# Kernel optimization log

Measured on AMD Instinct MI355X. Metric: run time of the kernel, lower is better.

The kernel has to match this reference:

```python
import jax, jax.numpy as jnp
import numpy as np

LUT_DIM = 33  # standard 33^3 color LUT


def setup_inputs() -> dict:
    key = jax.random.key(0)
    k1, k2 = jax.random.split(key)
    # learned 3D LUT: [out_channels=3, D_b, D_g, D_r]
    lut = jax.random.normal(k1, (3, LUT_DIM, LUT_DIM, LUT_DIM), dtype=jnp.float32) * 0.1
    # input image batch in [0, 1): [B, 3, H, W]
    x = jax.random.uniform(k2, (4, 3, 1024, 1024), dtype=jnp.float32)
    return {"lut": lut, "x": x}


def reference(lut, x):
    """Trilinear interpolation of a 3D color LUT (image-adaptive-3DLUT forward).

    lut: [3, D, D, D] laid out as lut[c, ib, ig, ir] (flat index ir + ig*D + ib*D*D)
    x:   [B, 3, H, W] with channels (r, g, b) in [0, 1]
    returns: [B, 3, H, W]
    """
    dim = lut.shape[-1]
    scale = dim - 1  # 1 / binsize

    r, g, b = x[:, 0], x[:, 1], x[:, 2]  # each [B, H, W]

    def cell(c):
        s = c * scale
        idx = jnp.clip(jnp.floor(s), 0, scale - 1).astype(jnp.int32)
        return idx, s - idx.astype(s.dtype)  # integer cell, fractional offset

    ir, dr = cell(r)
    ig, dg = cell(g)
    ib, db = cell(b)

    lut_flat = lut.reshape(3, -1)  # [3, D^3], tiny and cache-resident

    out = jnp.zeros((3,) + r.shape, dtype=x.dtype)  # [3, B, H, W]
    # 8 corners of the enclosing LUT cell, trilinear weights
    for or_ in (0, 1):
        wr = dr if or_ else (1.0 - dr)
        for og in (0, 1):
            wg = dg if og else (1.0 - dg)
            for ob in (0, 1):
                wb = db if ob else (1.0 - db)
                flat = ((ib + ob) * dim + (ig + og)) * dim + (ir + or_)  # [B, H, W]
                corner = lut_flat[:, flat]  # gather -> [3, B, H, W]
                out = out + (wr * wg * wb)[None] * corner

    return jnp.transpose(out, (1, 0, 2, 3))  # [B, 3, H, W]
```

## Files before the change

### kernel.cpp

```cpp
#include <hip/hip_runtime.h>
#include <hip/hip_fp16.h>


#define LUT_D     33
#define LUT_DD    (LUT_D * LUT_D)
#define LUT_N     (LUT_D * LUT_D * LUT_D)
#define CH_STRIDE 35940
#define STAGE_G   (CH_STRIDE / 4)
#define HW4       (1024 * 1024 / 4)
#define NGROUPS   (4 * HW4)
#define NCHUNKS   256
#define THREADS   1024
#define ITERS     (NGROUPS / NCHUNKS / THREADS)

typedef float vfloat4 __attribute__((ext_vector_type(4)));

__device__ __forceinline__ unsigned int pack2(float a, float b) {
    union { __half2 h; unsigned int u; } cv;
    cv.h = __floats2half2_rn(a, b);
    return cv.u;
}
__device__ __forceinline__ float2 unpack2(unsigned int p) {
    union { unsigned int u; __half2 h; } cv;
    cv.u = p;
    return __half22float2(cv.h);
}

__global__ __launch_bounds__(256)
void lut_pack_kernel(const float* __restrict__ lut, unsigned int* __restrict__ W) {
    const int t = blockIdx.x * 256 + (int)threadIdx.x;
    if (t >= 3 * LUT_N) return;
    const int c = t / LUT_N;
    const int i = t - c * LUT_N;
    const float a = lut[t];
    const float b = (i + LUT_DD < LUT_N) ? lut[t + LUT_DD] : 0.0f;
    W[c * CH_STRIDE + i] = pack2(a, b);
}

__global__ __launch_bounds__(THREADS)
void lut3d_trilerp_kernel(const unsigned int* __restrict__ Wsrc,
                          const float* __restrict__ x,
                          float* __restrict__ out) {
    extern __shared__ __align__(16) unsigned int W[];

    const int t  = (int)threadIdx.x;
    const int g0 = (int)blockIdx.x * (NGROUPS / NCHUNKS) + t;

    const float4* x4 = (const float4*)x;
    float4*       o4 = (float4*)out;

    auto stage = [&](int c) {
#pragma unroll
        for (int s = 0; s < 9; ++s) {
            const int gid = s * THREADS + t;
            if (gid < STAGE_G) {
                __builtin_amdgcn_global_load_lds(
                    (const __attribute__((address_space(1))) void*)(Wsrc + c * CH_STRIDE + gid * 4),
                    (__attribute__((address_space(3))) void*)(W + gid * 4),
                    16, 0, 0);
            }
        }
    };

    auto quad = [&](const int idx[4], const float dr4[4], const float dg4[4],
                    const float db4[4], int obase) {
        unsigned int q00[4], q01[4], q10[4], q11[4];
#pragma unroll
        for (int k = 0; k < 4; ++k) {
            q00[k] = W[idx[k]];
            q01[k] = W[idx[k] + 1];
            q10[k] = W[idx[k] + LUT_D];
            q11[k] = W[idx[k] + LUT_D + 1];
        }
        float oo[4];
#pragma unroll
        for (int k = 0; k < 4; ++k) {
            const float2 a = unpack2(q00[k]);
            const float2 b = unpack2(q01[k]);
            const float2 c = unpack2(q10[k]);
            const float2 d = unpack2(q11[k]);
            const float v00 = a.x + db4[k] * (a.y - a.x);
            const float v01 = b.x + db4[k] * (b.y - b.x);
            const float v10 = c.x + db4[k] * (c.y - c.x);
            const float v11 = d.x + db4[k] * (d.y - d.x);
            const float v0  = v00 + dr4[k] * (v01 - v00);
            const float v1  = v10 + dr4[k] * (v11 - v10);
            oo[k] = v0 + dg4[k] * (v1 - v0);
        }
        vfloat4 v = {oo[0], oo[1], oo[2], oo[3]};
        __builtin_nontemporal_store(v, (vfloat4*)&o4[obase]);
    };

    stage(0);
    int    ibs[ITERS];
    float4 R[ITERS], G[ITERS], B[ITERS];
    {
        const int bi = g0 >> 18, hw4 = g0 & (HW4 - 1);
        ibs[0] = bi * 3 * HW4 + hw4;
        R[0] = x4[ibs[0]];
        G[0] = x4[ibs[0] + HW4];
        B[0] = x4[ibs[0] + 2 * HW4];
    }
    __syncthreads();

    unsigned int pidx[ITERS][2], pdr[ITERS][2], pdg[ITERS][2], pdb[ITERS][2];

#pragma unroll
    for (int it = 0; it < ITERS; ++it) {
        if (it + 1 < ITERS) {
            const int g  = g0 + (it + 1) * THREADS;
            const int bi = g >> 18, hw4 = g & (HW4 - 1);
            ibs[it + 1] = bi * 3 * HW4 + hw4;
            R[it + 1] = x4[ibs[it + 1]];
            G[it + 1] = x4[ibs[it + 1] + HW4];
            B[it + 1] = x4[ibs[it + 1] + 2 * HW4];
        }
        const float rr[4] = {R[it].x, R[it].y, R[it].z, R[it].w};
        const float gw[4] = {G[it].x, G[it].y, G[it].z, G[it].w};
        const float bw[4] = {B[it].x, B[it].y, B[it].z, B[it].w};

        int idx[4]; float dr4[4], dg4[4], db4[4];
#pragma unroll
        for (int k = 0; k < 4; ++k) {
            const float sr = rr[k] * 32.0f;
            const float sg = gw[k] * 32.0f;
            const float sb = bw[k] * 32.0f;
            const float fr = fminf(fmaxf(floorf(sr), 0.0f), 31.0f);
            const float fg = fminf(fmaxf(floorf(sg), 0.0f), 31.0f);
            const float fb = fminf(fmaxf(floorf(sb), 0.0f), 31.0f);
            dr4[k] = sr - fr;
            dg4[k] = sg - fg;
            db4[k] = sb - fb;
            idx[k] = ((int)fb * LUT_D + (int)fg) * LUT_D + (int)fr;
        }
        pidx[it][0] = (unsigned)idx[0] | ((unsigned)idx[1] << 16);
        pidx[it][1] = (unsigned)idx[2] | ((unsigned)idx[3] << 16);
        pdr[it][0] = pack2(dr4[0], dr4[1]);  pdr[it][1] = pack2(dr4[2], dr4[3]);
        pdg[it][0] = pack2(dg4[0], dg4[1]);  pdg[it][1] = pack2(dg4[2], dg4[3]);
        pdb[it][0] = pack2(db4[0], db4[1]);  pdb[it][1] = pack2(db4[2], db4[3]);

        quad(idx, dr4, dg4, db4, ibs[it]);
    }

#pragma unroll
    for (int c = 1; c < 3; ++c) {
        __syncthreads();
        stage(c);
        __syncthreads();

#pragma unroll
        for (int it = 0; it < ITERS; ++it) {
            const int idx[4] = {(int)(pidx[it][0] & 0xffffu), (int)(pidx[it][0] >> 16),
                                (int)(pidx[it][1] & 0xffffu), (int)(pidx[it][1] >> 16)};
            const float2 r0 = unpack2(pdr[it][0]), r1 = unpack2(pdr[it][1]);
            const float2 gg = unpack2(pdg[it][0]), g1 = unpack2(pdg[it][1]);
            const float2 b0 = unpack2(pdb[it][0]), b1 = unpack2(pdb[it][1]);
            const float dr4[4] = {r0.x, r0.y, r1.x, r1.y};
            const float dg4[4] = {gg.x, gg.y, g1.x, g1.y};
            const float db4[4] = {b0.x, b0.y, b1.x, b1.y};
            quad(idx, dr4, dg4, db4, ibs[it] + c * HW4);
        }
    }
}

extern "C" void kernel_launch(void* const* d_in, const int* in_sizes, int n_in,
                              void* d_out, int out_size, void* d_ws, size_t ws_size,
                              hipStream_t stream) {
    const float*  lut = (const float*)d_in[0];
    const float*  x   = (const float*)d_in[1];
    float*        out = (float*)d_out;
    unsigned int* W   = (unsigned int*)d_ws;

    const int pack_grid = (3 * LUT_N + 255) / 256;
    lut_pack_kernel<<<pack_grid, 256, 0, stream>>>(lut, W);

    const size_t lds_bytes = (size_t)CH_STRIDE * 4;
    lut3d_trilerp_kernel<<<NCHUNKS, THREADS, lds_bytes, stream>>>(W, x, out);
}
```

Measured before the change: 117.0 us.

## Pair LUT along r axis, issue all input loads upfront, keep fp32 coords in registers

Packs each LUT entry with its r-neighbour instead of its b-neighbour and reorders the trilinear lerps to match. All input pixel loads are now issued at once after staging, with a partial vmcnt wait and a raw s_barrier instead of a one-ahead prefetch. Per-pixel indices and fractions stay in fp32 and int registers rather than being packed to half, which removes the pack and unpack work and improves precision but raises register pressure. The vmcnt(12) wait assumes a particular ordering of outstanding loads, so correctness depends on the compiler's instruction order.

```diff
diff --git a/kernel.cpp b/kernel.cpp
--- a/kernel.cpp
+++ b/kernel.cpp
@@ -33,7 +33,7 @@
     const int c = t / LUT_N;
     const int i = t - c * LUT_N;
     const float a = lut[t];
-    const float b = (i + LUT_DD < LUT_N) ? lut[t + LUT_DD] : 0.0f;
+    const float b = (i + 1 < LUT_N) ? lut[t + 1] : 0.0f;
     W[c * CH_STRIDE + i] = pack2(a, b);
 }
 
@@ -68,58 +68,55 @@
 #pragma unroll
         for (int k = 0; k < 4; ++k) {
             q00[k] = W[idx[k]];
-            q01[k] = W[idx[k] + 1];
-            q10[k] = W[idx[k] + LUT_D];
-            q11[k] = W[idx[k] + LUT_D + 1];
+            q01[k] = W[idx[k] + LUT_D];
+            q10[k] = W[idx[k] + LUT_DD];
+            q11[k] = W[idx[k] + LUT_DD + LUT_D];
         }
         float oo[4];
 #pragma unroll
         for (int k = 0; k < 4; ++k) {
-            const float2 a = unpack2(q00[k]);
-            const float2 b = unpack2(q01[k]);
-            const float2 c = unpack2(q10[k]);
-            const float2 d = unpack2(q11[k]);
-            const float v00 = a.x + db4[k] * (a.y - a.x);
-            const float v01 = b.x + db4[k] * (b.y - b.x);
-            const float v10 = c.x + db4[k] * (c.y - c.x);
-            const float v11 = d.x + db4[k] * (d.y - d.x);
-            const float v0  = v00 + dr4[k] * (v01 - v00);
-            const float v1  = v10 + dr4[k] * (v11 - v10);
-            oo[k] = v0 + dg4[k] * (v1 - v0);
+            const float2 a00 = unpack2(q00[k]);
+            const float2 a01 = unpack2(q01[k]);
+            const float2 a10 = unpack2(q10[k]);
+            const float2 a11 = unpack2(q11[k]);
+            const float l00 = a00.x + dr4[k] * (a00.y - a00.x);
+            const float l01 = a01.x + dr4[k] * (a01.y - a01.x);
+            const float l10 = a10.x + dr4[k] * (a10.y - a10.x);
+            const float l11 = a11.x + dr4[k] * (a11.y - a11.x);
+            const float l0  = l00 + dg4[k] * (l01 - l00);
+            const float l1  = l10 + dg4[k] * (l11 - l10);
+            oo[k] = l0 + db4[k] * (l1 - l0);
         }
         vfloat4 v = {oo[0], oo[1], oo[2], oo[3]};
         __builtin_nontemporal_store(v, (vfloat4*)&o4[obase]);
     };
 
     stage(0);
+    __builtin_amdgcn_sched_barrier(0);
+
     int    ibs[ITERS];
     float4 R[ITERS], G[ITERS], B[ITERS];
-    {
-        const int bi = g0 >> 18, hw4 = g0 & (HW4 - 1);
-        ibs[0] = bi * 3 * HW4 + hw4;
-        R[0] = x4[ibs[0]];
-        G[0] = x4[ibs[0] + HW4];
-        B[0] = x4[ibs[0] + 2 * HW4];
-    }
-    __syncthreads();
-
-    unsigned int pidx[ITERS][2], pdr[ITERS][2], pdg[ITERS][2], pdb[ITERS][2];
-
 #pragma unroll
     for (int it = 0; it < ITERS; ++it) {
-        if (it + 1 < ITERS) {
-            const int g  = g0 + (it + 1) * THREADS;
-            const int bi = g >> 18, hw4 = g & (HW4 - 1);
-            ibs[it + 1] = bi * 3 * HW4 + hw4;
-            R[it + 1] = x4[ibs[it + 1]];
-            G[it + 1] = x4[ibs[it + 1] + HW4];
-            B[it + 1] = x4[ibs[it + 1] + 2 * HW4];
-        }
+        const int g  = g0 + it * THREADS;
+        const int bi = g >> 18, hw4 = g & (HW4 - 1);
+        ibs[it] = bi * 3 * HW4 + hw4;
+        R[it] = x4[ibs[it]];
+        G[it] = x4[ibs[it] + HW4];
+        B[it] = x4[ibs[it] + 2 * HW4];
+    }
+    __builtin_amdgcn_sched_barrier(0);
+    asm volatile("s_waitcnt vmcnt(12)" ::: "memory");
+    __builtin_amdgcn_s_barrier();
+    __builtin_amdgcn_sched_barrier(0);
+
+    int   idx[ITERS][4];
+    float dr[ITERS][4], dg[ITERS][4], db[ITERS][4];
+#pragma unroll
+    for (int it = 0; it < ITERS; ++it) {
         const float rr[4] = {R[it].x, R[it].y, R[it].z, R[it].w};
         const float gw[4] = {G[it].x, G[it].y, G[it].z, G[it].w};
         const float bw[4] = {B[it].x, B[it].y, B[it].z, B[it].w};
-
-        int idx[4]; float dr4[4], dg4[4], db4[4];
 #pragma unroll
         for (int k = 0; k < 4; ++k) {
             const float sr = rr[k] * 32.0f;
@@ -128,18 +125,12 @@
             const float fr = fminf(fmaxf(floorf(sr), 0.0f), 31.0f);
             const float fg = fminf(fmaxf(floorf(sg), 0.0f), 31.0f);
             const float fb = fminf(fmaxf(floorf(sb), 0.0f), 31.0f);
-            dr4[k] = sr - fr;
-            dg4[k] = sg - fg;
-            db4[k] = sb - fb;
-            idx[k] = ((int)fb * LUT_D + (int)fg) * LUT_D + (int)fr;
+            dr[it][k] = sr - fr;
+            dg[it][k] = sg - fg;
+            db[it][k] = sb - fb;
+            idx[it][k] = ((int)fb * LUT_D + (int)fg) * LUT_D + (int)fr;
         }
-        pidx[it][0] = (unsigned)idx[0] | ((unsigned)idx[1] << 16);
-        pidx[it][1] = (unsigned)idx[2] | ((unsigned)idx[3] << 16);
-        pdr[it][0] = pack2(dr4[0], dr4[1]);  pdr[it][1] = pack2(dr4[2], dr4[3]);
-        pdg[it][0] = pack2(dg4[0], dg4[1]);  pdg[it][1] = pack2(dg4[2], dg4[3]);
-        pdb[it][0] = pack2(db4[0], db4[1]);  pdb[it][1] = pack2(db4[2], db4[3]);
-
-        quad(idx, dr4, dg4, db4, ibs[it]);
+        quad(idx[it], dr[it], dg[it], db[it], ibs[it]);
     }
 
 #pragma unroll
@@ -147,18 +138,9 @@
         __syncthreads();
         stage(c);
         __syncthreads();
-
 #pragma unroll
         for (int it = 0; it < ITERS; ++it) {
-            const int idx[4] = {(int)(pidx[it][0] & 0xffffu), (int)(pidx[it][0] >> 16),
-                                (int)(pidx[it][1] & 0xffffu), (int)(pidx[it][1] >> 16)};
-            const float2 r0 = unpack2(pdr[it][0]), r1 = unpack2(pdr[it][1]);
-            const float2 gg = unpack2(pdg[it][0]), g1 = unpack2(pdg[it][1]);
-            const float2 b0 = unpack2(pdb[it][0]), b1 = unpack2(pdb[it][1]);
-            const float dr4[4] = {r0.x, r0.y, r1.x, r1.y};
-            const float dg4[4] = {gg.x, gg.y, g1.x, g1.y};
-            const float db4[4] = {b0.x, b0.y, b1.x, b1.y};
-            quad(idx, dr4, dg4, db4, ibs[it] + c * HW4);
+            quad(idx[it], dr[it], dg[it], db[it], ibs[it] + c * HW4);
         }
     }
 }
```

Measured after the change: 114.1 us. 1.03x faster.
